# Kernel tuning notes

Hardware: AMD Instinct MI355X
Metric: run time of the kernel (lower is better)

## Reference

```python
import jax, jax.numpy as jnp
import numpy as np

T, B, D_IN, D_H, D_OUT, RANK = 512, 64, 128, 1024, 256, 64


def setup_inputs() -> dict:
    key = jax.random.key(0)
    ks = jax.random.split(key, 7)
    return {
        "x": jax.random.normal(ks[0], (T, B, D_IN), dtype=jnp.float32),
        "Wi": jax.random.normal(ks[1], (D_H, D_IN), dtype=jnp.float32) / np.sqrt(D_IN).astype(np.float32),
        "U": jax.random.normal(ks[2], (D_H, RANK), dtype=jnp.float32) / np.sqrt(RANK).astype(np.float32),
        "V": jax.random.normal(ks[3], (RANK, D_H), dtype=jnp.float32) / np.sqrt(D_H).astype(np.float32),
        "bh": jax.random.normal(ks[4], (D_H,), dtype=jnp.float32),
        "Wo": jax.random.normal(ks[5], (D_OUT, D_H), dtype=jnp.float32) / np.sqrt(D_H).astype(np.float32),
        "bo": jax.random.normal(ks[6], (D_OUT,), dtype=jnp.float32),
    }


def reference(x, Wi, U, V, bh, Wo, bo):
    # i2h projections for all timesteps at once (no recurrence on input path)
    zi = jnp.einsum('tbi,hi->tbh', x, Wi)  # [T, B, D_H]

    def step(h, zi_t):
        # h2h low-rank: weight = U @ V, so h @ W.T = (h @ V.T) @ U.T
        h_new = jax.nn.relu((h @ V.T) @ U.T + bh + zi_t)
        return h_new, h_new

    h0 = jnp.zeros((x.shape[1], Wi.shape[0]), dtype=x.dtype)
    _, hidden = jax.lax.scan(step, h0, zi)  # hidden: [T, B, D_H]
    output = hidden @ Wo.T + bo  # [T, B, D_OUT]
    return hidden, output
```

## Files before the change

### kernel.cpp

```cpp
#include <hip/hip_runtime.h>

#define T_STEPS 512
#define B_SZ    64
#define DIN     128
#define DH      1024
#define DOUT    256
#define RNK     64
#define HID_ELEMS ((size_t)T_STEPS * B_SZ * DH)

typedef _Float16 h2  __attribute__((ext_vector_type(2)));
typedef _Float16 h8v __attribute__((ext_vector_type(8)));
typedef short    s8v __attribute__((ext_vector_type(8)));
typedef float    f4v __attribute__((ext_vector_type(4)));

#define WGBAR() asm volatile("s_waitcnt lgkmcnt(0)\n\ts_barrier" ::: "memory")

static __device__ __forceinline__ unsigned short f2bf(float f) {
    unsigned u = __float_as_uint(f);
    unsigned r = (u + 0x7FFFu + ((u >> 16) & 1u)) >> 16;
    return (unsigned short)r;
}

__global__ __launch_bounds__(256) void k0_cvt(
    const float* __restrict__ Wo, unsigned short* __restrict__ Wo16)
{
    int i = (blockIdx.x * 256 + threadIdx.x) * 4;
    float4 v = *reinterpret_cast<const float4*>(&Wo[i]);
    ushort4 o;
    o.x = f2bf(v.x); o.y = f2bf(v.y); o.z = f2bf(v.z); o.w = f2bf(v.w);
    *reinterpret_cast<ushort4*>(&Wo16[i]) = o;
}

__global__ __launch_bounds__(256) void k1_zi(
    const float* __restrict__ x, const float* __restrict__ Wi,
    const float* __restrict__ bh, float* __restrict__ zi)
{
    __shared__ float At[64][68];
    __shared__ float Bt[64][68];
    const int m0 = blockIdx.y * 64;
    const int n0 = blockIdx.x * 64;
    const int tid = threadIdx.x;
    const int tx = tid & 15, ty = tid >> 4;
    float acc[4][4] = {};

    for (int kc = 0; kc < DIN; kc += 64) {
        #pragma unroll
        for (int i = 0; i < 4; ++i) {
            int idx = tid + i * 256;
            int row = idx >> 4;
            int c4  = idx & 15;
            float4 v = *reinterpret_cast<const float4*>(&x[(size_t)(m0 + row) * DIN + kc + c4 * 4]);
            At[c4*4+0][row] = v.x; At[c4*4+1][row] = v.y;
            At[c4*4+2][row] = v.z; At[c4*4+3][row] = v.w;
        }
        #pragma unroll
        for (int i = 0; i < 4; ++i) {
            int idx = tid + i * 256;
            int row = idx >> 4;
            int c4  = idx & 15;
            float4 v = *reinterpret_cast<const float4*>(&Wi[(size_t)(n0 + row) * DIN + kc + c4 * 4]);
            Bt[c4*4+0][row] = v.x; Bt[c4*4+1][row] = v.y;
            Bt[c4*4+2][row] = v.z; Bt[c4*4+3][row] = v.w;
        }
        __syncthreads();
        #pragma unroll
        for (int k = 0; k < 64; ++k) {
            float4 a = *reinterpret_cast<const float4*>(&At[k][ty * 4]);
            float4 b = *reinterpret_cast<const float4*>(&Bt[k][tx * 4]);
            float av[4] = {a.x, a.y, a.z, a.w};
            float bv[4] = {b.x, b.y, b.z, b.w};
            #pragma unroll
            for (int i = 0; i < 4; ++i)
                #pragma unroll
                for (int j = 0; j < 4; ++j)
                    acc[i][j] = fmaf(av[i], bv[j], acc[i][j]);
        }
        __syncthreads();
    }
    float4 bias = *reinterpret_cast<const float4*>(&bh[n0 + tx * 4]);
    #pragma unroll
    for (int i = 0; i < 4; ++i) {
        float4 o;
        o.x = acc[i][0] + bias.x; o.y = acc[i][1] + bias.y;
        o.z = acc[i][2] + bias.z; o.w = acc[i][3] + bias.w;
        *reinterpret_cast<float4*>(&zi[(size_t)(m0 + ty * 4 + i) * DH + n0 + tx * 4]) = o;
    }
}

__global__ __launch_bounds__(512, 1) void k2_rec(
    const float* __restrict__ U, const float* __restrict__ V,
    float* __restrict__ hid)
{
    __shared__ _Float16 h16[DH];
    __shared__ float red[8][64];
    const int b    = blockIdx.x;
    const int tid  = threadIdx.x;
    const int lane = tid & 63;
    const int g    = tid >> 6;
    const int j0   = tid, j1 = tid + 512;

    float u0[64], u1[64];
    const float4* __restrict__ U4 = reinterpret_cast<const float4*>(U);
    #pragma unroll
    for (int q = 0; q < 16; ++q) {
        float4 a = U4[j0 * 16 + q];
        u0[q*4+0]=a.x; u0[q*4+1]=a.y; u0[q*4+2]=a.z; u0[q*4+3]=a.w;
        float4 c = U4[j1 * 16 + q];
        u1[q*4+0]=c.x; u1[q*4+1]=c.y; u1[q*4+2]=c.z; u1[q*4+3]=c.w;
    }
    h2 vh[64];
    {
        const float2* __restrict__ vrow =
            reinterpret_cast<const float2*>(V + (size_t)lane * DH + g * 128);
        #pragma unroll
        for (int m = 0; m < 64; ++m) {
            float2 f = vrow[m];
            h2 p; p.x = (_Float16)f.x; p.y = (_Float16)f.y;
            vh[m] = p;
        }
    }

    float rv = 0.0f;
    size_t base = (size_t)b * DH;
    float z0 = hid[base + j0];
    float z1 = hid[base + j1];

    for (int t = 0; t < T_STEPS; ++t) {
        float e0p[4] = {z0, 0.f, 0.f, 0.f};
        float e1p[4] = {z1, 0.f, 0.f, 0.f};
        #pragma unroll
        for (int kk = 0; kk < 64; ++kk) {
            float rk = __uint_as_float(__builtin_amdgcn_readlane(__float_as_uint(rv), kk));
            e0p[kk & 3] = fmaf(rk, u0[kk], e0p[kk & 3]);
            e1p[kk & 3] = fmaf(rk, u1[kk], e1p[kk & 3]);
        }
        float h0 = fmaxf((e0p[0] + e0p[1]) + (e0p[2] + e0p[3]), 0.0f);
        float h1 = fmaxf((e1p[0] + e1p[1]) + (e1p[2] + e1p[3]), 0.0f);

        size_t nbase = base + (size_t)B_SZ * DH;
        float nz0 = hid[nbase + j0];
        float nz1 = hid[nbase + j1];

        hid[base + j0] = h0;
        hid[base + j1] = h1;
        h16[j0] = (_Float16)h0;
        h16[j1] = (_Float16)h1;

        WGBAR();

        float ap[4] = {0.f, 0.f, 0.f, 0.f};
        const h8v* __restrict__ hp8 = reinterpret_cast<const h8v*>(&h16[g * 128]);
        #pragma unroll
        for (int q = 0; q < 16; ++q) {
            h8v hv = hp8[q];
            h2 p0; p0.x = hv[0]; p0.y = hv[1];
            h2 p1; p1.x = hv[2]; p1.y = hv[3];
            h2 p2; p2.x = hv[4]; p2.y = hv[5];
            h2 p3; p3.x = hv[6]; p3.y = hv[7];
            ap[0] = __builtin_amdgcn_fdot2(p0, vh[q*4+0], ap[0], false);
            ap[1] = __builtin_amdgcn_fdot2(p1, vh[q*4+1], ap[1], false);
            ap[2] = __builtin_amdgcn_fdot2(p2, vh[q*4+2], ap[2], false);
            ap[3] = __builtin_amdgcn_fdot2(p3, vh[q*4+3], ap[3], false);
        }
        red[g][lane] = (ap[0] + ap[1]) + (ap[2] + ap[3]);

        WGBAR();

        rv = ((red[0][lane] + red[1][lane]) + (red[2][lane] + red[3][lane]))
           + ((red[4][lane] + red[5][lane]) + (red[6][lane] + red[7][lane]));
        z0 = nz0; z1 = nz1;
        base = nbase;
    }
}

__global__ __launch_bounds__(256, 1) void k3_out(
    const float* __restrict__ hid, const unsigned short* __restrict__ Wo16,
    const float* __restrict__ bo, float* __restrict__ out)
{
    __shared__ unsigned short As[128][72];
    __shared__ unsigned short Bs[128][72];
    const int tid = threadIdx.x;
    const int w  = tid >> 6, l = tid & 63;
    const int wr = w >> 1,  wc = w & 1;
    const int m0 = blockIdx.x * 128;
    const int n0 = blockIdx.y * 128;
    const int fr = l & 15;
    const int fg = l >> 4;
    f4v acc[4][4] = {};

    for (int kc = 0; kc < DH; kc += 64) {
        __syncthreads();
        #pragma unroll
        for (int uu = 0; uu < 4; ++uu) {
            int u = tid + uu * 256;
            int row = u >> 3, ks = u & 7;
            const float4* src = reinterpret_cast<const float4*>(
                &hid[(size_t)(m0 + row) * DH + kc + ks * 8]);
            float4 a = src[0], bqq = src[1];
            s8v t;
            t[0] = (short)f2bf(a.x);  t[1] = (short)f2bf(a.y);
            t[2] = (short)f2bf(a.z);  t[3] = (short)f2bf(a.w);
            t[4] = (short)f2bf(bqq.x); t[5] = (short)f2bf(bqq.y);
            t[6] = (short)f2bf(bqq.z); t[7] = (short)f2bf(bqq.w);
            *reinterpret_cast<s8v*>(&As[row][ks * 8]) = t;
        }
        #pragma unroll
        for (int uu = 0; uu < 4; ++uu) {
            int u = tid + uu * 256;
            int row = u >> 3, ks = u & 7;
            s8v v = *reinterpret_cast<const s8v*>(
                &Wo16[(size_t)(n0 + row) * DH + kc + ks * 8]);
            *reinterpret_cast<s8v*>(&Bs[row][ks * 8]) = v;
        }
        __syncthreads();
        #pragma unroll
        for (int kk = 0; kk < 64; kk += 32) {
            s8v af[4], bf[4];
            #pragma unroll
            for (int i = 0; i < 4; ++i)
                af[i] = *reinterpret_cast<const s8v*>(&As[wr*64 + i*16 + fr][kk + fg*8]);
            #pragma unroll
            for (int i = 0; i < 4; ++i)
                bf[i] = *reinterpret_cast<const s8v*>(&Bs[wc*64 + i*16 + fr][kk + fg*8]);
            #pragma unroll
            for (int mi = 0; mi < 4; ++mi)
                #pragma unroll
                for (int ni = 0; ni < 4; ++ni)
                    acc[mi][ni] = __builtin_amdgcn_mfma_f32_16x16x32_bf16(
                        af[mi], bf[ni], acc[mi][ni], 0, 0, 0);
        }
    }
    #pragma unroll
    for (int ni = 0; ni < 4; ++ni) {
        int col = n0 + wc*64 + ni*16 + fr;
        float bias = bo[col];
        #pragma unroll
        for (int mi = 0; mi < 4; ++mi) {
            #pragma unroll
            for (int r = 0; r < 4; ++r) {
                int row = m0 + wr*64 + mi*16 + fg*4 + r;
                out[(size_t)row * DOUT + col] = acc[mi][ni][r] + bias;
            }
        }
    }
}

extern "C" void kernel_launch(void* const* d_in, const int* in_sizes, int n_in,
                              void* d_out, int out_size, void* d_ws, size_t ws_size,
                              hipStream_t stream)
{
    const float* x  = (const float*)d_in[0];
    const float* Wi = (const float*)d_in[1];
    const float* U  = (const float*)d_in[2];
    const float* V  = (const float*)d_in[3];
    const float* bh = (const float*)d_in[4];
    const float* Wo = (const float*)d_in[5];
    const float* bo = (const float*)d_in[6];
    float* hid  = (float*)d_out;
    float* outp = (float*)d_out + HID_ELEMS;
    unsigned short* Wo16 = (unsigned short*)d_ws;

    k0_cvt<<<dim3(DOUT * DH / (256 * 4)), 256, 0, stream>>>(Wo, Wo16);
    k1_zi<<<dim3(DH / 64, (T_STEPS * B_SZ) / 64), 256, 0, stream>>>(x, Wi, bh, hid);
    k2_rec<<<dim3(B_SZ), 512, 0, stream>>>(U, V, hid);
    k3_out<<<dim3((T_STEPS * B_SZ) / 128, DOUT / 128), 256, 0, stream>>>(hid, Wo16, bo, outp);
}
```

Before: 998.6 us.

## Use 1024-thread recurrence blocks with one unit per thread and one barrier per step

The recurrent kernel now launches 1024 threads per batch row, so each thread owns one hidden unit instead of two, and each wave covers 64 hidden columns of the V projection. Each wave now reads only the h16 slice it wrote itself, so the first workgroup barrier is replaced by a local LDS wait. The reduction buffer is double-buffered by step parity so the single remaining barrier is enough. This halves the serial FMA and dot work per thread on each step's critical path and removes one barrier per step. In exchange the reduction has 16 partial sums instead of 8, and four waves share each SIMD, which can limit how much the per-step latency actually drops.

```diff
diff --git a/kernel.cpp b/kernel.cpp
--- a/kernel.cpp
+++ b/kernel.cpp
@@ -21,6 +21,10 @@
     return (unsigned short)r;
 }
 
+static __device__ __forceinline__ float rdlane(float v, int l) {
+    return __uint_as_float(__builtin_amdgcn_readlane(__float_as_uint(v), l));
+}
+
 __global__ __launch_bounds__(256) void k0_cvt(
     const float* __restrict__ Wo, unsigned short* __restrict__ Wo16)
 {
@@ -87,33 +91,31 @@
     }
 }
 
-__global__ __launch_bounds__(512, 1) void k2_rec(
+__global__ __launch_bounds__(1024, 1) void k2_rec(
     const float* __restrict__ U, const float* __restrict__ V,
     float* __restrict__ hid)
 {
     __shared__ _Float16 h16[DH];
-    __shared__ float red[8][64];
+    __shared__ float red[2][16][64];
     const int b    = blockIdx.x;
     const int tid  = threadIdx.x;
     const int lane = tid & 63;
     const int g    = tid >> 6;
-    const int j0   = tid, j1 = tid + 512;
-
-    float u0[64], u1[64];
+    const int j    = tid;
+
+    float u[64];
     const float4* __restrict__ U4 = reinterpret_cast<const float4*>(U);
     #pragma unroll
     for (int q = 0; q < 16; ++q) {
-        float4 a = U4[j0 * 16 + q];
-        u0[q*4+0]=a.x; u0[q*4+1]=a.y; u0[q*4+2]=a.z; u0[q*4+3]=a.w;
-        float4 c = U4[j1 * 16 + q];
-        u1[q*4+0]=c.x; u1[q*4+1]=c.y; u1[q*4+2]=c.z; u1[q*4+3]=c.w;
-    }
-    h2 vh[64];
+        float4 a = U4[j * 16 + q];
+        u[q*4+0]=a.x; u[q*4+1]=a.y; u[q*4+2]=a.z; u[q*4+3]=a.w;
+    }
+    h2 vh[32];
     {
         const float2* __restrict__ vrow =
-            reinterpret_cast<const float2*>(V + (size_t)lane * DH + g * 128);
-        #pragma unroll
-        for (int m = 0; m < 64; ++m) {
+            reinterpret_cast<const float2*>(V + (size_t)lane * DH + g * 64);
+        #pragma unroll
+        for (int m = 0; m < 32; ++m) {
             float2 f = vrow[m];
             h2 p; p.x = (_Float16)f.x; p.y = (_Float16)f.y;
             vh[m] = p;
@@ -122,54 +124,60 @@
 
     float rv = 0.0f;
     size_t base = (size_t)b * DH;
-    float z0 = hid[base + j0];
-    float z1 = hid[base + j1];
+    float z = hid[base + j];
 
     for (int t = 0; t < T_STEPS; ++t) {
-        float e0p[4] = {z0, 0.f, 0.f, 0.f};
-        float e1p[4] = {z1, 0.f, 0.f, 0.f};
-        #pragma unroll
-        for (int kk = 0; kk < 64; ++kk) {
-            float rk = __uint_as_float(__builtin_amdgcn_readlane(__float_as_uint(rv), kk));
-            e0p[kk & 3] = fmaf(rk, u0[kk], e0p[kk & 3]);
-            e1p[kk & 3] = fmaf(rk, u1[kk], e1p[kk & 3]);
-        }
-        float h0 = fmaxf((e0p[0] + e0p[1]) + (e0p[2] + e0p[3]), 0.0f);
-        float h1 = fmaxf((e1p[0] + e1p[1]) + (e1p[2] + e1p[3]), 0.0f);
+        float e0 = z, e1 = 0.f, e2 = 0.f, e3 = 0.f;
+        #pragma unroll
+        for (int kk = 0; kk < 64; kk += 4) {
+            float r0 = rdlane(rv, kk + 0);
+            float r1 = rdlane(rv, kk + 1);
+            float r2 = rdlane(rv, kk + 2);
+            float r3 = rdlane(rv, kk + 3);
+            e0 = fmaf(r0, u[kk + 0], e0);
+            e1 = fmaf(r1, u[kk + 1], e1);
+            e2 = fmaf(r2, u[kk + 2], e2);
+            e3 = fmaf(r3, u[kk + 3], e3);
+        }
+        float h = fmaxf((e0 + e1) + (e2 + e3), 0.0f);
 
         size_t nbase = base + (size_t)B_SZ * DH;
-        float nz0 = hid[nbase + j0];
-        float nz1 = hid[nbase + j1];
-
-        hid[base + j0] = h0;
-        hid[base + j1] = h1;
-        h16[j0] = (_Float16)h0;
-        h16[j1] = (_Float16)h1;
-
-        WGBAR();
-
-        float ap[4] = {0.f, 0.f, 0.f, 0.f};
-        const h8v* __restrict__ hp8 = reinterpret_cast<const h8v*>(&h16[g * 128]);
-        #pragma unroll
-        for (int q = 0; q < 16; ++q) {
+        float nz = hid[nbase + j];
+        hid[base + j] = h;
+        h16[j] = (_Float16)h;
+
+        asm volatile("s_waitcnt lgkmcnt(0)" ::: "memory");
+
+        float a0 = 0.f, a1 = 0.f, a2 = 0.f, a3 = 0.f;
+        const h8v* __restrict__ hp8 = reinterpret_cast<const h8v*>(&h16[g * 64]);
+        #pragma unroll
+        for (int q = 0; q < 8; ++q) {
             h8v hv = hp8[q];
             h2 p0; p0.x = hv[0]; p0.y = hv[1];
             h2 p1; p1.x = hv[2]; p1.y = hv[3];
             h2 p2; p2.x = hv[4]; p2.y = hv[5];
             h2 p3; p3.x = hv[6]; p3.y = hv[7];
-            ap[0] = __builtin_amdgcn_fdot2(p0, vh[q*4+0], ap[0], false);
-            ap[1] = __builtin_amdgcn_fdot2(p1, vh[q*4+1], ap[1], false);
-            ap[2] = __builtin_amdgcn_fdot2(p2, vh[q*4+2], ap[2], false);
-            ap[3] = __builtin_amdgcn_fdot2(p3, vh[q*4+3], ap[3], false);
-        }
-        red[g][lane] = (ap[0] + ap[1]) + (ap[2] + ap[3]);
+            a0 = __builtin_amdgcn_fdot2(p0, vh[q*4+0], a0, false);
+            a1 = __builtin_amdgcn_fdot2(p1, vh[q*4+1], a1, false);
+            a2 = __builtin_amdgcn_fdot2(p2, vh[q*4+2], a2, false);
+            a3 = __builtin_amdgcn_fdot2(p3, vh[q*4+3], a3, false);
+        }
+        red[t & 1][g][lane] = (a0 + a1) + (a2 + a3);
 
         WGBAR();
 
-        rv = ((red[0][lane] + red[1][lane]) + (red[2][lane] + red[3][lane]))
-           + ((red[4][lane] + red[5][lane]) + (red[6][lane] + red[7][lane]));
-        z0 = nz0; z1 = nz1;
-        base = nbase;
+        const float* __restrict__ rr = &red[t & 1][0][0];
+        float s0 = rr[ 0*64 + lane] + rr[ 1*64 + lane];
+        float s1 = rr[ 2*64 + lane] + rr[ 3*64 + lane];
+        float s2 = rr[ 4*64 + lane] + rr[ 5*64 + lane];
+        float s3 = rr[ 6*64 + lane] + rr[ 7*64 + lane];
+        float s4 = rr[ 8*64 + lane] + rr[ 9*64 + lane];
+        float s5 = rr[10*64 + lane] + rr[11*64 + lane];
+        float s6 = rr[12*64 + lane] + rr[13*64 + lane];
+        float s7 = rr[14*64 + lane] + rr[15*64 + lane];
+        rv = ((s0 + s1) + (s2 + s3)) + ((s4 + s5) + (s6 + s7));
+
+        z = nz; base = nbase;
     }
 }
 
@@ -262,6 +270,6 @@
 
     k0_cvt<<<dim3(DOUT * DH / (256 * 4)), 256, 0, stream>>>(Wo, Wo16);
     k1_zi<<<dim3(DH / 64, (T_STEPS * B_SZ) / 64), 256, 0, stream>>>(x, Wi, bh, hid);
-    k2_rec<<<dim3(B_SZ), 512, 0, stream>>>(U, V, hid);
+    k2_rec<<<dim3(B_SZ), 1024, 0, stream>>>(U, V, hid);
     k3_out<<<dim3((T_STEPS * B_SZ) / 128, DOUT / 128), 256, 0, stream>>>(hid, Wo16, bo, outp);
 }
```

Result: slower. 1.090 ms (+9.2%).
